# Kernel optimization log

Measured on AMD Instinct MI355X. Metric: run time of the kernel, lower is better.

Reference implementation:

```python
import jax, jax.numpy as jnp
import numpy as np

INF = 1.0e10
EPS = 1e-12

def setup_inputs() -> dict:
    key = jax.random.key(0)
    k1, k2 = jax.random.split(key)
    B, N, A = 512, 16384, 64
    return {
        "residue_ca_pos": jax.random.normal(k1, (B, N, 3), dtype=jnp.float32) * 10.0,
        "residue_mask": jnp.ones((B, N), dtype=jnp.float32),
        "atom_pos": jax.random.normal(k2, (B, A, 3), dtype=jnp.float32) * 10.0,
        "atom_mask": jnp.ones((B, A), dtype=jnp.float32),
        "max_p": 1,
        "top_k": 4096,
    }

def reference(residue_ca_pos, residue_mask, atom_pos, atom_mask, max_p, top_k):
    # ligand centroid per batch: [B, 3]
    centroid = atom_pos.sum(-2) / atom_mask.sum(-1, keepdims=True)
    # distance from centroid to each residue Ca, invalid residues pushed to +inf
    diff = centroid[:, None, :] - residue_ca_pos            # [B, N, 3]
    dists = jnp.sqrt(jnp.sum(diff * diff, axis=-1) + EPS) + (1.0 - residue_mask) * INF
    # k smallest distances -> neighbor indices [B, top_k]
    _, nbr_indices = jax.lax.top_k(-dists, top_k)
    rows = jnp.arange(residue_mask.shape[0])[:, None]       # [B, 1]
    # scatter writes building the masks (faithful to torch scatter_ with constants)
    residue_spatial_mask = residue_mask.at[rows, nbr_indices].set(0.0)
    residue_spatial_mask_esm = (1.0 - residue_mask).at[rows, nbr_indices].set(32.0)
    return residue_spatial_mask, residue_spatial_mask_esm
```

## Files before the change

kernel.cpp:

```cpp
#include <hip/hip_runtime.h>

#pragma clang fp contract(off)

#define B_   512
#define N_   16384
#define A_   64
#define TPB  1024
#define CAP  2048

__global__ __launch_bounds__(256) void centroid_kernel(
    const float* __restrict__ atom_pos, const float* __restrict__ atom_mask,
    float* __restrict__ cent)
{
#pragma clang fp contract(off)
    int b = blockIdx.x * blockDim.x + threadIdx.x;
    if (b >= B_) return;
    const float* ap = atom_pos + (size_t)b * A_ * 3;
    const float* am = atom_mask + (size_t)b * A_;

    float sx = ap[0], sy = ap[1], sz = ap[2];
    for (int a = 1; a < A_; ++a) {
        sx += ap[a * 3 + 0];
        sy += ap[a * 3 + 1];
        sz += ap[a * 3 + 2];
    }

    float r0 = am[0], r1 = am[1], r2 = am[2], r3 = am[3];
    float r4 = am[4], r5 = am[5], r6 = am[6], r7 = am[7];
    for (int i = 8; i < A_; i += 8) {
        r0 += am[i + 0]; r1 += am[i + 1]; r2 += am[i + 2]; r3 += am[i + 3];
        r4 += am[i + 4]; r5 += am[i + 5]; r6 += am[i + 6]; r7 += am[i + 7];
    }
    float ms = ((r0 + r1) + (r2 + r3)) + ((r4 + r5) + (r6 + r7));

    cent[b * 4 + 0] = sx / ms;
    cent[b * 4 + 1] = sy / ms;
    cent[b * 4 + 2] = sz / ms;
}

__global__ __launch_bounds__(TPB) void select_kernel(
    const float* __restrict__ pos, const float* __restrict__ mask,
    const int* __restrict__ topk_ptr, const float* __restrict__ cent,
    float* __restrict__ out0, float* __restrict__ out1)
{
#pragma clang fp contract(off)
    __shared__ unsigned short dist16[N_];
    __shared__ unsigned       hist[2048];
    __shared__ unsigned       hist2[32];
    __shared__ unsigned       wsum[64];
    __shared__ unsigned       cand_bits[CAP];
    __shared__ unsigned short cand_idx[CAP];
    __shared__ float          s_c[3];
    __shared__ unsigned       s_B11, s_less11, s_P16, s_j, s_ncand, s_k;

    const int tid = threadIdx.x;
    const int b   = blockIdx.x;
    const float* __restrict__ p = pos  + (size_t)b * N_ * 3;
    const float* __restrict__ m = mask + (size_t)b * N_;

    for (int i = tid; i < 2048; i += TPB) hist[i] = 0u;
    if (tid < 32) hist2[tid] = 0u;
    if (tid == 0) {
        s_ncand = 0u;
        s_c[0] = cent[b * 4 + 0];
        s_c[1] = cent[b * 4 + 1];
        s_c[2] = cent[b * 4 + 2];
        int k = *topk_ptr;
        if (k < 0)  k = 0;
        if (k > N_) k = N_;
        s_k = (unsigned)k;
    }
    __syncthreads();

    const float cx = s_c[0], cy = s_c[1], cz = s_c[2];
    const unsigned k = s_k;

    for (int i = tid; i < N_; i += TPB) {
        float px = p[i * 3 + 0], py = p[i * 3 + 1], pz = p[i * 3 + 2];
        float dx = cx - px, dy = cy - py, dz = cz - pz;
        float dx2 = dx * dx, dy2 = dy * dy, dz2 = dz * dz;
        float s = (dx2 + dy2) + dz2;
        s = s + 1e-12f;
        float d = sqrtf(s);
        float im = (1.0f - m[i]) * 1e10f;
        d = d + im;
        unsigned bits = __float_as_uint(d);
        dist16[i] = (unsigned short)(bits >> 16);
        atomicAdd(&hist[bits >> 21], 1u);
    }
    __syncthreads();

    if (k > 0) {
        if (tid < 64) {
            unsigned s = 0; const int base = tid * 32;
            for (int i = 0; i < 32; ++i) s += hist[base + i];
            wsum[tid] = s;
        }
        __syncthreads();
        if (tid == 0) {
            unsigned cum = 0; int g = 63;
            for (int t = 0; t < 64; ++t) {
                if (cum + wsum[t] >= k) { g = t; break; }
                cum += wsum[t];
            }
            int b11 = g * 32 + 31;
            for (int i = 0; i < 32; ++i) {
                unsigned h = hist[g * 32 + i];
                if (cum + h >= k) { b11 = g * 32 + i; break; }
                cum += h;
            }
            s_B11 = (unsigned)b11; s_less11 = cum;
        }
        __syncthreads();
        const unsigned B11 = s_B11;

        for (int i = tid; i < N_; i += TPB) {
            unsigned v = dist16[i];
            if ((v >> 5) == B11) atomicAdd(&hist2[v & 31u], 1u);
        }
        __syncthreads();
        if (tid == 0) {
            unsigned cum = s_less11; int sb = 31;
            for (int i = 0; i < 32; ++i) {
                unsigned h = hist2[i];
                if (cum + h >= k) { sb = i; break; }
                cum += h;
            }
            s_P16 = (B11 << 5) | (unsigned)sb;
            s_j   = k - cum;
        }
        __syncthreads();
        const unsigned P16 = s_P16;
        const unsigned j   = s_j;

        for (int i = tid; i < N_; i += TPB) {
            if (dist16[i] == (unsigned short)P16) {
                unsigned w = atomicAdd(&s_ncand, 1u);
                if (w < CAP) {
                    float px = p[i * 3 + 0], py = p[i * 3 + 1], pz = p[i * 3 + 2];
                    float dx = cx - px, dy = cy - py, dz = cz - pz;
                    float dx2 = dx * dx, dy2 = dy * dy, dz2 = dz * dz;
                    float s = (dx2 + dy2) + dz2;
                    s = s + 1e-12f;
                    float d = sqrtf(s);
                    float im = (1.0f - m[i]) * 1e10f;
                    d = d + im;
                    cand_bits[w] = __float_as_uint(d);
                    cand_idx[w]  = (unsigned short)i;
                }
            }
        }
        __syncthreads();

        const unsigned c = min(s_ncand, (unsigned)CAP);
        for (unsigned t = tid; t < c; t += TPB) {
            unsigned bt = cand_bits[t];
            unsigned it = cand_idx[t];
            unsigned rank = 0;
            for (unsigned u = 0; u < c; ++u) {
                unsigned bu = cand_bits[u];
                rank += (bu < bt) || (bu == bt && (unsigned)cand_idx[u] < it);
            }
            if (rank < j) dist16[it] = 0;
        }
        __syncthreads();
    }

    const unsigned P16f = (k > 0) ? s_P16 : 0u;
    for (int i = tid; i < N_; i += TPB) {
        bool sel = (k > 0) && ((unsigned)dist16[i] < P16f);
        float mv = m[i];
        out0[(size_t)b * N_ + i] = sel ? 0.0f  : mv;
        out1[(size_t)b * N_ + i] = sel ? 32.0f : (1.0f - mv);
    }
}

extern "C" void kernel_launch(void* const* d_in, const int* in_sizes, int n_in,
                              void* d_out, int out_size, void* d_ws, size_t ws_size,
                              hipStream_t stream) {
    const float* pos   = (const float*)d_in[0];
    const float* rmask = (const float*)d_in[1];
    const float* apos  = (const float*)d_in[2];
    const float* amask = (const float*)d_in[3];
    const int*   topk  = (const int*)d_in[5];

    float* out0 = (float*)d_out;
    float* out1 = out0 + (size_t)B_ * N_;
    float* cent = (float*)d_ws;

    centroid_kernel<<<(B_ + 255) / 256, 256, 0, stream>>>(apos, amask, cent);
    select_kernel<<<B_, TPB, 0, stream>>>(pos, rmask, topk, cent, out0, out1);
}
```

Baseline: 227.9 us.

## Fuse centroid into select kernel, keep distances in registers, vectorize IO

Merges the centroid computation into the per-batch select kernel, which removes one launch and the workspace round trip. Distances and mask values are kept in registers across phases, so the later histogram, candidate and output passes no longer reread global memory or recompute distances. Loads and stores are vectorized with float4/ushort4, and the serial prefix scans are replaced with wave-level shuffle scans and ballots. Register pressure rises at 1024 threads per block, and the final output pass now skips the k>0 check.

Result: faster. 210.7 us (-7.6%).

```diff
diff --git a/kernel.cpp b/kernel.cpp
--- a/kernel.cpp
+++ b/kernel.cpp
@@ -7,49 +7,21 @@
 #define A_   64
 #define TPB  1024
 #define CAP  2048
-
-__global__ __launch_bounds__(256) void centroid_kernel(
-    const float* __restrict__ atom_pos, const float* __restrict__ atom_mask,
-    float* __restrict__ cent)
-{
-#pragma clang fp contract(off)
-    int b = blockIdx.x * blockDim.x + threadIdx.x;
-    if (b >= B_) return;
-    const float* ap = atom_pos + (size_t)b * A_ * 3;
-    const float* am = atom_mask + (size_t)b * A_;
-
-    float sx = ap[0], sy = ap[1], sz = ap[2];
-    for (int a = 1; a < A_; ++a) {
-        sx += ap[a * 3 + 0];
-        sy += ap[a * 3 + 1];
-        sz += ap[a * 3 + 2];
-    }
-
-    float r0 = am[0], r1 = am[1], r2 = am[2], r3 = am[3];
-    float r4 = am[4], r5 = am[5], r6 = am[6], r7 = am[7];
-    for (int i = 8; i < A_; i += 8) {
-        r0 += am[i + 0]; r1 += am[i + 1]; r2 += am[i + 2]; r3 += am[i + 3];
-        r4 += am[i + 4]; r5 += am[i + 5]; r6 += am[i + 6]; r7 += am[i + 7];
-    }
-    float ms = ((r0 + r1) + (r2 + r3)) + ((r4 + r5) + (r6 + r7));
-
-    cent[b * 4 + 0] = sx / ms;
-    cent[b * 4 + 1] = sy / ms;
-    cent[b * 4 + 2] = sz / ms;
-}
-
-__global__ __launch_bounds__(TPB) void select_kernel(
-    const float* __restrict__ pos, const float* __restrict__ mask,
-    const int* __restrict__ topk_ptr, const float* __restrict__ cent,
+#define ITERS 4
+
+__global__ __launch_bounds__(TPB) void fused_kernel(
+    const float* __restrict__ pos,   const float* __restrict__ mask,
+    const float* __restrict__ apos,  const float* __restrict__ amask,
+    const int*   __restrict__ topk_ptr,
     float* __restrict__ out0, float* __restrict__ out1)
 {
 #pragma clang fp contract(off)
     __shared__ unsigned short dist16[N_];
     __shared__ unsigned       hist[2048];
     __shared__ unsigned       hist2[32];
-    __shared__ unsigned       wsum[64];
     __shared__ unsigned       cand_bits[CAP];
     __shared__ unsigned short cand_idx[CAP];
+    __shared__ float          s_atoms[A_ * 3 + A_];
     __shared__ float          s_c[3];
     __shared__ unsigned       s_B11, s_less11, s_P16, s_j, s_ncand, s_k;
 
@@ -58,95 +30,143 @@
     const float* __restrict__ p = pos  + (size_t)b * N_ * 3;
     const float* __restrict__ m = mask + (size_t)b * N_;
 
-    for (int i = tid; i < 2048; i += TPB) hist[i] = 0u;
+    hist[tid]        = 0u;
+    hist[tid + 1024] = 0u;
     if (tid < 32) hist2[tid] = 0u;
+    if (tid < 256)
+        s_atoms[tid] = (tid < 192) ? apos[(size_t)b * 192 + tid]
+                                   : amask[(size_t)b * 64 + (tid - 192)];
     if (tid == 0) {
         s_ncand = 0u;
-        s_c[0] = cent[b * 4 + 0];
-        s_c[1] = cent[b * 4 + 1];
-        s_c[2] = cent[b * 4 + 2];
-        int k = *topk_ptr;
-        if (k < 0)  k = 0;
-        if (k > N_) k = N_;
-        s_k = (unsigned)k;
+        int kk = *topk_ptr;
+        if (kk < 0)  kk = 0;
+        if (kk > N_) kk = N_;
+        s_k = (unsigned)kk;
+    }
+    __syncthreads();
+
+    if (tid < 64) {
+        float comp = 0.0f, ms = 0.0f;
+        if (tid < 3) {
+            comp = s_atoms[tid];
+            for (int a = 1; a < A_; ++a) comp += s_atoms[a * 3 + tid];
+        }
+        if (tid == 3) {
+            const float* am = s_atoms + 192;
+            float r0 = am[0], r1 = am[1], r2 = am[2], r3 = am[3];
+            float r4 = am[4], r5 = am[5], r6 = am[6], r7 = am[7];
+            for (int i = 8; i < A_; i += 8) {
+                r0 += am[i + 0]; r1 += am[i + 1]; r2 += am[i + 2]; r3 += am[i + 3];
+                r4 += am[i + 4]; r5 += am[i + 5]; r6 += am[i + 6]; r7 += am[i + 7];
+            }
+            ms = ((r0 + r1) + (r2 + r3)) + ((r4 + r5) + (r6 + r7));
+        }
+        ms = __shfl(ms, 3, 64);
+        if (tid < 3) s_c[tid] = comp / ms;
     }
     __syncthreads();
 
     const float cx = s_c[0], cy = s_c[1], cz = s_c[2];
     const unsigned k = s_k;
 
-    for (int i = tid; i < N_; i += TPB) {
-        float px = p[i * 3 + 0], py = p[i * 3 + 1], pz = p[i * 3 + 2];
-        float dx = cx - px, dy = cy - py, dz = cz - pz;
-        float dx2 = dx * dx, dy2 = dy * dy, dz2 = dz * dz;
-        float s = (dx2 + dy2) + dz2;
-        s = s + 1e-12f;
-        float d = sqrtf(s);
-        float im = (1.0f - m[i]) * 1e10f;
-        d = d + im;
-        unsigned bits = __float_as_uint(d);
-        dist16[i] = (unsigned short)(bits >> 16);
-        atomicAdd(&hist[bits >> 21], 1u);
+    unsigned rbits[ITERS * 4];
+    float    rm[ITERS * 4];
+#pragma unroll
+    for (int it = 0; it < ITERS; ++it) {
+        const int i0 = it * (TPB * 4) + tid * 4;
+        const float4 pa = *(const float4*)(p + (size_t)i0 * 3);
+        const float4 pb = *(const float4*)(p + (size_t)i0 * 3 + 4);
+        const float4 pc = *(const float4*)(p + (size_t)i0 * 3 + 8);
+        const float4 mv = *(const float4*)(m + i0);
+        const float px[4] = {pa.x, pa.w, pb.z, pc.y};
+        const float py[4] = {pa.y, pb.x, pb.w, pc.z};
+        const float pz[4] = {pa.z, pb.y, pc.x, pc.w};
+        const float mm[4] = {mv.x, mv.y, mv.z, mv.w};
+        unsigned short loc[4];
+#pragma unroll
+        for (int j = 0; j < 4; ++j) {
+            float dx = cx - px[j], dy = cy - py[j], dz = cz - pz[j];
+            float dx2 = dx * dx, dy2 = dy * dy, dz2 = dz * dz;
+            float s = (dx2 + dy2) + dz2;
+            s = s + 1e-12f;
+            float d = sqrtf(s);
+            float im = (1.0f - mm[j]) * 1e10f;
+            d = d + im;
+            const unsigned bits = __float_as_uint(d);
+            rbits[it * 4 + j] = bits;
+            rm[it * 4 + j]    = mm[j];
+            loc[j] = (unsigned short)(bits >> 16);
+            atomicAdd(&hist[bits >> 21], 1u);
+        }
+        *(ushort4*)&dist16[i0] = make_ushort4(loc[0], loc[1], loc[2], loc[3]);
     }
     __syncthreads();
 
     if (k > 0) {
         if (tid < 64) {
-            unsigned s = 0; const int base = tid * 32;
-            for (int i = 0; i < 32; ++i) s += hist[base + i];
-            wsum[tid] = s;
-        }
-        __syncthreads();
-        if (tid == 0) {
-            unsigned cum = 0; int g = 63;
-            for (int t = 0; t < 64; ++t) {
-                if (cum + wsum[t] >= k) { g = t; break; }
-                cum += wsum[t];
-            }
-            int b11 = g * 32 + 31;
-            for (int i = 0; i < 32; ++i) {
-                unsigned h = hist[g * 32 + i];
-                if (cum + h >= k) { b11 = g * 32 + i; break; }
-                cum += h;
-            }
-            s_B11 = (unsigned)b11; s_less11 = cum;
+            unsigned s = 0;
+#pragma unroll
+            for (int i = 0; i < 32; ++i) s += hist[tid * 32 + i];
+            unsigned incl = s;
+#pragma unroll
+            for (int off = 1; off < 64; off <<= 1) {
+                unsigned v = (unsigned)__shfl_up((int)incl, off, 64);
+                if (tid >= off) incl += v;
+            }
+            unsigned long long bal = __ballot(incl >= k);
+            const int g = __ffsll(bal) - 1;
+            const unsigned cum1 = (unsigned)__shfl((int)(incl - s), g, 64);
+
+            unsigned h2 = (tid < 32) ? hist[g * 32 + tid] : 0u;
+            unsigned incl2 = h2;
+#pragma unroll
+            for (int off = 1; off < 64; off <<= 1) {
+                unsigned v = (unsigned)__shfl_up((int)incl2, off, 64);
+                if (tid >= off) incl2 += v;
+            }
+            unsigned long long bal2 = __ballot(tid < 32 && (cum1 + incl2 >= k));
+            const int sb = __ffsll(bal2) - 1;
+            const unsigned cum2 = cum1 + (unsigned)__shfl((int)(incl2 - h2), sb, 64);
+            if (tid == 0) { s_B11 = (unsigned)(g * 32 + sb); s_less11 = cum2; }
         }
         __syncthreads();
         const unsigned B11 = s_B11;
 
-        for (int i = tid; i < N_; i += TPB) {
-            unsigned v = dist16[i];
+#pragma unroll
+        for (int x = 0; x < ITERS * 4; ++x) {
+            const unsigned v = rbits[x] >> 16;
             if ((v >> 5) == B11) atomicAdd(&hist2[v & 31u], 1u);
         }
         __syncthreads();
-        if (tid == 0) {
-            unsigned cum = s_less11; int sb = 31;
-            for (int i = 0; i < 32; ++i) {
-                unsigned h = hist2[i];
-                if (cum + h >= k) { sb = i; break; }
-                cum += h;
-            }
-            s_P16 = (B11 << 5) | (unsigned)sb;
-            s_j   = k - cum;
+        if (tid < 64) {
+            unsigned h = (tid < 32) ? hist2[tid] : 0u;
+            unsigned incl = h;
+#pragma unroll
+            for (int off = 1; off < 64; off <<= 1) {
+                unsigned v = (unsigned)__shfl_up((int)incl, off, 64);
+                if (tid >= off) incl += v;
+            }
+            const unsigned less11 = s_less11;
+            unsigned long long bal = __ballot(tid < 32 && (less11 + incl >= k));
+            const int sb = __ffsll(bal) - 1;
+            const unsigned cumx = less11 + (unsigned)__shfl((int)(incl - h), sb, 64);
+            if (tid == 0) { s_P16 = (B11 << 5) | (unsigned)sb; s_j = k - cumx; }
         }
         __syncthreads();
         const unsigned P16 = s_P16;
         const unsigned j   = s_j;
 
-        for (int i = tid; i < N_; i += TPB) {
-            if (dist16[i] == (unsigned short)P16) {
-                unsigned w = atomicAdd(&s_ncand, 1u);
-                if (w < CAP) {
-                    float px = p[i * 3 + 0], py = p[i * 3 + 1], pz = p[i * 3 + 2];
-                    float dx = cx - px, dy = cy - py, dz = cz - pz;
-                    float dx2 = dx * dx, dy2 = dy * dy, dz2 = dz * dz;
-                    float s = (dx2 + dy2) + dz2;
-                    s = s + 1e-12f;
-                    float d = sqrtf(s);
-                    float im = (1.0f - m[i]) * 1e10f;
-                    d = d + im;
-                    cand_bits[w] = __float_as_uint(d);
-                    cand_idx[w]  = (unsigned short)i;
+#pragma unroll
+        for (int it = 0; it < ITERS; ++it) {
+#pragma unroll
+            for (int jj = 0; jj < 4; ++jj) {
+                const unsigned bits = rbits[it * 4 + jj];
+                if ((bits >> 16) == P16) {
+                    const unsigned w = atomicAdd(&s_ncand, 1u);
+                    if (w < CAP) {
+                        cand_bits[w] = bits;
+                        cand_idx[w]  = (unsigned short)(it * (TPB * 4) + tid * 4 + jj);
+                    }
                 }
             }
         }
@@ -154,11 +174,11 @@
 
         const unsigned c = min(s_ncand, (unsigned)CAP);
         for (unsigned t = tid; t < c; t += TPB) {
-            unsigned bt = cand_bits[t];
-            unsigned it = cand_idx[t];
+            const unsigned bt = cand_bits[t];
+            const unsigned it = cand_idx[t];
             unsigned rank = 0;
             for (unsigned u = 0; u < c; ++u) {
-                unsigned bu = cand_bits[u];
+                const unsigned bu = cand_bits[u];
                 rank += (bu < bt) || (bu == bt && (unsigned)cand_idx[u] < it);
             }
             if (rank < j) dist16[it] = 0;
@@ -167,11 +187,22 @@
     }
 
     const unsigned P16f = (k > 0) ? s_P16 : 0u;
-    for (int i = tid; i < N_; i += TPB) {
-        bool sel = (k > 0) && ((unsigned)dist16[i] < P16f);
-        float mv = m[i];
-        out0[(size_t)b * N_ + i] = sel ? 0.0f  : mv;
-        out1[(size_t)b * N_ + i] = sel ? 32.0f : (1.0f - mv);
+#pragma unroll
+    for (int it = 0; it < ITERS; ++it) {
+        const int i0 = it * (TPB * 4) + tid * 4;
+        const ushort4 dv = *(const ushort4*)&dist16[i0];
+        const unsigned short dvs[4] = {dv.x, dv.y, dv.z, dv.w};
+        float4 o0, o1;
+        float* o0p = &o0.x; float* o1p = &o1.x;
+#pragma unroll
+        for (int jj = 0; jj < 4; ++jj) {
+            const bool sel = (unsigned)dvs[jj] < P16f;
+            const float mv = rm[it * 4 + jj];
+            o0p[jj] = sel ? 0.0f  : mv;
+            o1p[jj] = sel ? 32.0f : (1.0f - mv);
+        }
+        *(float4*)(out0 + (size_t)b * N_ + i0) = o0;
+        *(float4*)(out1 + (size_t)b * N_ + i0) = o1;
     }
 }
 
@@ -186,8 +217,6 @@
 
     float* out0 = (float*)d_out;
     float* out1 = out0 + (size_t)B_ * N_;
-    float* cent = (float*)d_ws;
-
-    centroid_kernel<<<(B_ + 255) / 256, 256, 0, stream>>>(apos, amask, cent);
-    select_kernel<<<B_, TPB, 0, stream>>>(pos, rmask, topk, cent, out0, out1);
+
+    fused_kernel<<<B_, TPB, 0, stream>>>(pos, rmask, apos, amask, topk, out0, out1);
 }
```
